# Performance work log

Hardware: AMD Instinct MI355X
Metric: run time of the kernel (lower is better)

Reference implementation:

```python
import jax, jax.numpy as jnp
import numpy as np

WIN = 8  # window_size from init_kwargs


def setup_inputs() -> dict:
    key = jax.random.key(0)
    k1, k2, k3 = jax.random.split(key, 3)
    B, H, W, C = 8, 128, 128, 384
    x = jax.random.normal(k1, (B, H * W, C), dtype=jnp.float32)
    w_qkv = jax.random.normal(k2, (C, 3 * C), dtype=jnp.float32) * 0.02
    b_qkv = jnp.zeros((3 * C,), dtype=jnp.float32)
    w_proj = jax.random.normal(k3, (C, C), dtype=jnp.float32) * 0.02
    b_proj = jnp.zeros((C,), dtype=jnp.float32)
    return {"x": x, "w_qkv": w_qkv, "b_qkv": b_qkv,
            "w_proj": w_proj, "b_proj": b_proj, "h": H, "w": W}


def reference(x, w_qkv, b_qkv, w_proj, b_proj, h, w):
    B = x.shape[0]
    C = x.shape[-1]
    win = WIN
    xs = x.reshape(B, h, w, C)
    pad_h = (-h) % win
    pad_w = (-w) % win
    xp = jnp.pad(xs, ((0, 0), (0, pad_h), (0, pad_w), (0, 0)))
    hp, wp = h + pad_h, w + pad_w
    xw = xp.reshape(B, hp // win, win, wp // win, win, C)
    xw = xw.transpose(0, 1, 3, 2, 4, 5).reshape(B, -1, win * win, C)
    qkv = xw @ w_qkv + b_qkv
    q, k, v = jnp.split(qkv, 3, axis=-1)
    # NOTE: original has no 1/sqrt(d) scaling and no head split (num_heads unused)
    attn = jax.nn.softmax(jnp.einsum('bnqc,bnkc->bnqk', q, k), axis=-1)
    out = jnp.einsum('bnqk,bnkc->bnqc', attn, v)
    out = out @ w_proj + b_proj
    # reverse window partition
    out = out.reshape(B, hp // win, wp // win, win, win, C)
    out = out.transpose(0, 1, 3, 2, 4, 5).reshape(B, hp, wp, C)
    out = out[:, :h, :w, :].reshape(B, h * w, C)
    return out
```

## Files before the change

### kernel.cpp

```cpp
#include <hip/hip_runtime.h>
#include <stdint.h>

typedef unsigned short u16;
typedef __attribute__((ext_vector_type(8))) short bf16x8;
typedef __attribute__((ext_vector_type(4))) short bf16x4;
typedef __attribute__((ext_vector_type(4))) float f32x4;

#define MFMA(A,B,C) __builtin_amdgcn_mfma_f32_16x16x32_bf16((A),(B),(C),0,0,0)

__device__ __forceinline__ u16 f2bf(float f) {
  uint32_t u = __float_as_uint(f);
  return (u16)((u + 0x7fffu + ((u >> 16) & 1u)) >> 16);
}

__device__ __forceinline__ void async16(u16* lds, const u16* g) {
  __builtin_amdgcn_global_load_lds(
      (const __attribute__((address_space(1))) uint32_t*)g,
      (__attribute__((address_space(3))) uint32_t*)lds, 16, 0, 0);
}

__global__ void k_prep(const float* __restrict__ wqkv, const float* __restrict__ wproj,
                       u16* __restrict__ wqkvP, u16* __restrict__ wprojT)
{
  int i = blockIdx.x * 256 + threadIdx.x;
  if (i < 384 * 1152) {
    int kg = i / 9216; int rem = i - kg * 9216; int n = rem >> 3; int t = rem & 7;
    wqkvP[i] = (u16)f2bf(wqkv[(kg * 8 + t) * 1152 + n]);
  }
  if (i < 384 * 384) {
    int co = i / 384, c = i - co * 384;
    wprojT[i] = (u16)f2bf(wproj[c * 384 + co]);
  }
}

__global__ __launch_bounds__(512, 4)
void k_qkv(const float* __restrict__ x, const u16* __restrict__ wp,
           const float* __restrict__ bqkv,
           u16* __restrict__ Qb, u16* __restrict__ Kbuf, u16* __restrict__ Vt)
{
  __shared__ alignas(16) u16 sA[64 * 392];
  const int tid = threadIdx.x;
  const int win = blockIdx.x;
  const int bb = win >> 8, wy = (win >> 4) & 15, wx = win & 15;

  {
    int r = tid >> 3, c0 = (tid & 7) * 48;
    int tok = (wy * 8 + (r >> 3)) * 128 + wx * 8 + (r & 7);
    const float* src = x + (size_t)(bb * 16384 + tok) * 384 + c0;
    u16* dst = &sA[r * 392 + c0];
#pragma unroll
    for (int j = 0; j < 6; ++j) {
      f32x4 a0 = *(const f32x4*)(src + j * 8);
      f32x4 a1 = *(const f32x4*)(src + j * 8 + 4);
      bf16x8 w;
#pragma unroll
      for (int e = 0; e < 4; ++e) { w[e] = (short)f2bf(a0[e]); w[e + 4] = (short)f2bf(a1[e]); }
      *(bf16x8*)(dst + j * 8) = w;
    }
  }
  __syncthreads();

  const int lane = tid & 63, l15 = lane & 15, l4 = lane >> 4;
  const int wn = tid >> 6;
  const u16* bB = wp + l4 * 9216 + (size_t)(wn * 48 + l15) * 8;
  const f32x4 z4 = {0.f, 0.f, 0.f, 0.f};

#pragma unroll
  for (int nt = 0; nt < 3; ++nt) {
    f32x4 acc[4][3];
#pragma unroll
    for (int mf = 0; mf < 4; ++mf)
#pragma unroll
      for (int nf = 0; nf < 3; ++nf) acc[mf][nf] = z4;
    const u16* bp = bB + nt * 3072;

    if (nt < 2) {
#pragma unroll
      for (int t = 0; t < 12; ++t) {
        bf16x8 af[4], bfr[3];
#pragma unroll
        for (int mf = 0; mf < 4; ++mf)
          af[mf] = *(const bf16x8*)&sA[(mf * 16 + l15) * 392 + t * 32 + l4 * 8];
#pragma unroll
        for (int nf = 0; nf < 3; ++nf)
          bfr[nf] = *(const bf16x8*)(bp + (size_t)t * 36864 + nf * 128);
#pragma unroll
        for (int mf = 0; mf < 4; ++mf)
#pragma unroll
          for (int nf = 0; nf < 3; ++nf)
            acc[mf][nf] = MFMA(bfr[nf], af[mf], acc[mf][nf]);
      }
      u16* dst = (nt == 0) ? Qb : Kbuf;
      f32x4 bias[3];
#pragma unroll
      for (int nf = 0; nf < 3; ++nf)
        bias[nf] = *(const f32x4*)&bqkv[nt * 384 + wn * 48 + nf * 16 + l4 * 4];
#pragma unroll
      for (int mf = 0; mf < 4; ++mf) {
        int row = mf * 16 + l15;
        char* rp = (char*)(dst + (size_t)(win * 64 + row) * 384);
        int sw = (nt == 1) ? ((row & 7) << 4) : 0;
#pragma unroll
        for (int nf = 0; nf < 3; ++nf) {
          bf16x4 pk;
#pragma unroll
          for (int e = 0; e < 4; ++e) pk[e] = (short)f2bf(acc[mf][nf][e] + bias[nf][e]);
          *(bf16x4*)(rp + ((wn * 96 + nf * 32 + l4 * 8) ^ sw)) = pk;
        }
      }
    } else {
#pragma unroll
      for (int t = 0; t < 12; ++t) {
        bf16x8 af[4], bfr[3];
#pragma unroll
        for (int mf = 0; mf < 4; ++mf)
          af[mf] = *(const bf16x8*)&sA[(mf * 16 + l15) * 392 + t * 32 + l4 * 8];
#pragma unroll
        for (int nf = 0; nf < 3; ++nf)
          bfr[nf] = *(const bf16x8*)(bp + (size_t)t * 36864 + nf * 128);
#pragma unroll
        for (int mf = 0; mf < 4; ++mf)
#pragma unroll
          for (int nf = 0; nf < 3; ++nf)
            acc[mf][nf] = MFMA(af[mf], bfr[nf], acc[mf][nf]);
      }
      float bv[3];
#pragma unroll
      for (int nf = 0; nf < 3; ++nf) bv[nf] = bqkv[768 + wn * 48 + nf * 16 + l15];
#pragma unroll
      for (int mf = 0; mf < 4; ++mf) {
        int key = mf * 16 + l4 * 4;
#pragma unroll
        for (int nf = 0; nf < 3; ++nf) {
          int c = wn * 48 + nf * 16 + l15;
          bf16x4 pk;
#pragma unroll
          for (int e = 0; e < 4; ++e) pk[e] = (short)f2bf(acc[mf][nf][e] + bv[nf]);
          *(bf16x4*)&Vt[((size_t)win * 384 + c) * 64 + key] = pk;
        }
      }
    }
  }
}

__global__ __launch_bounds__(256, 2)
void k_attn(const u16* __restrict__ Qb, const u16* __restrict__ Kbuf,
            const u16* __restrict__ Vt, const u16* __restrict__ WpT,
            const float* __restrict__ bproj, float* __restrict__ out)
{
  __shared__ alignas(16) u16 sKO[64 * 392];
  __shared__ alignas(16) u16 sP[64 * 64];
  __shared__ float sD[64];
  const int win = blockIdx.x;
  const int tid = threadIdx.x, wid = tid >> 6;
  const int lane = tid & 63, l15 = lane & 15, l4 = lane >> 4;
  const int swz = (l15 & 7) << 4;
  const f32x4 z4 = {0.f, 0.f, 0.f, 0.f};

  bf16x8 qa[12];
  const u16* qp = Qb + (size_t)(win * 64 + wid * 16 + l15) * 384 + l4 * 8;
#pragma unroll
  for (int cb = 0; cb < 12; ++cb) qa[cb] = *(const bf16x8*)(qp + cb * 32);
  bf16x8 vfr[6][2];
  const u16* vp = Vt + ((size_t)win * 384 + wid * 96 + l15) * 64 + l4 * 8;
#pragma unroll
  for (int nf = 0; nf < 6; ++nf)
#pragma unroll
    for (int ks = 0; ks < 2; ++ks)
      vfr[nf][ks] = *(const bf16x8*)(vp + nf * 1024 + ks * 32);
  const u16* kg = Kbuf + (size_t)win * 64 * 384;
#pragma unroll
  for (int t = 0; t < 12; ++t)
    async16((u16*)sKO + (t * 256 + tid) * 8, kg + (size_t)(t * 256 + tid) * 8);
  __syncthreads();

  f32x4 s[4];
#pragma unroll
  for (int nf = 0; nf < 4; ++nf) s[nf] = z4;
#pragma unroll
  for (int cb = 0; cb < 12; ++cb) {
#pragma unroll
    for (int nf = 0; nf < 4; ++nf) {
      bf16x8 kf = *(const bf16x8*)((char*)sKO +
                    (((nf * 16 + l15) * 768 + cb * 64 + l4 * 16) ^ swz));
      s[nf] = MFMA(kf, qa[cb], s[nf]);
    }
  }
  float mx = s[0][0];
#pragma unroll
  for (int nf = 0; nf < 4; ++nf)
#pragma unroll
    for (int e = 0; e < 4; ++e) mx = fmaxf(mx, s[nf][e]);
  mx = fmaxf(mx, __shfl_xor(mx, 16, 64));
  mx = fmaxf(mx, __shfl_xor(mx, 32, 64));
  float p[4][4], sum = 0.f;
#pragma unroll
  for (int nf = 0; nf < 4; ++nf)
#pragma unroll
    for (int e = 0; e < 4; ++e) { p[nf][e] = __expf(s[nf][e] - mx); sum += p[nf][e]; }
  sum += __shfl_xor(sum, 16, 64);
  sum += __shfl_xor(sum, 32, 64);
  const int q1 = wid * 16 + l15;
  if (lane < 16) sD[q1] = sum;
#pragma unroll
  for (int nf = 0; nf < 4; ++nf) {
    bf16x4 pk;
#pragma unroll
    for (int e = 0; e < 4; ++e) pk[e] = (short)f2bf(p[nf][e]);
    *(bf16x4*)((char*)sP + ((q1 * 128 + nf * 32 + l4 * 8) ^ swz)) = pk;
  }
  __syncthreads();

  bf16x8 pa[4][2];
#pragma unroll
  for (int mf = 0; mf < 4; ++mf)
#pragma unroll
    for (int ks = 0; ks < 2; ++ks)
      pa[mf][ks] = *(const bf16x8*)((char*)sP +
                     (((mf * 16 + l15) * 128 + ks * 64 + l4 * 16) ^ swz));
  f32x4 o[6][4];
#pragma unroll
  for (int nf = 0; nf < 6; ++nf)
#pragma unroll
    for (int mf = 0; mf < 4; ++mf) o[nf][mf] = z4;
#pragma unroll
  for (int nf = 0; nf < 6; ++nf)
#pragma unroll
    for (int ks = 0; ks < 2; ++ks)
#pragma unroll
      for (int mf = 0; mf < 4; ++mf)
        o[nf][mf] = MFMA(vfr[nf][ks], pa[mf][ks], o[nf][mf]);
#pragma unroll
  for (int nf = 0; nf < 6; ++nf)
#pragma unroll
    for (int mf = 0; mf < 4; ++mf) {
      bf16x4 pk;
#pragma unroll
      for (int e = 0; e < 4; ++e) pk[e] = (short)f2bf(o[nf][mf][e]);
      *(bf16x4*)((char*)sKO + ((mf * 16 + l15) * 784 + wid * 192 + nf * 32 + l4 * 8)) = pk;
    }
  __syncthreads();

  f32x4 pacc[6][4];
#pragma unroll
  for (int mf = 0; mf < 6; ++mf)
#pragma unroll
    for (int nf = 0; nf < 4; ++nf) pacc[mf][nf] = z4;
  const u16* wptr = WpT + (size_t)(wid * 96 + l15) * 384 + l4 * 8;
#pragma unroll
  for (int cb = 0; cb < 12; ++cb) {
    bf16x8 ob[4];
#pragma unroll
    for (int nf = 0; nf < 4; ++nf)
      ob[nf] = *(const bf16x8*)((char*)sKO + ((nf * 16 + l15) * 784 + cb * 64 + l4 * 16));
#pragma unroll
    for (int mf = 0; mf < 6; ++mf) {
      bf16x8 wf = *(const bf16x8*)(wptr + mf * 6144 + cb * 32);
#pragma unroll
      for (int nf = 0; nf < 4; ++nf)
        pacc[mf][nf] = MFMA(wf, ob[nf], pacc[mf][nf]);
    }
  }
  float rD[4];
#pragma unroll
  for (int nf = 0; nf < 4; ++nf) rD[nf] = 1.0f / sD[nf * 16 + l15];
  f32x4 bias[6];
#pragma unroll
  for (int mf = 0; mf < 6; ++mf) bias[mf] = *(const f32x4*)&bproj[wid * 96 + mf * 16 + l4 * 4];
  int bb = win >> 8, wy = (win >> 4) & 15, wx = win & 15;
#pragma unroll
  for (int nf = 0; nf < 4; ++nf) {
    int q = nf * 16 + l15;
    int tok = (wy * 8 + (q >> 3)) * 128 + wx * 8 + (q & 7);
    float* dst = out + (size_t)(bb * 16384 + tok) * 384 + wid * 96 + l4 * 4;
#pragma unroll
    for (int mf = 0; mf < 6; ++mf) {
      f32x4 v;
#pragma unroll
      for (int e = 0; e < 4; ++e) v[e] = pacc[mf][nf][e] * rD[nf] + bias[mf][e];
      *(f32x4*)(dst + mf * 16) = v;
    }
  }
}

extern "C" void kernel_launch(void* const* d_in, const int* in_sizes, int n_in,
                              void* d_out, int out_size, void* d_ws, size_t ws_size,
                              hipStream_t stream) {
  const float* x     = (const float*)d_in[0];
  const float* wqkv  = (const float*)d_in[1];
  const float* bqkv  = (const float*)d_in[2];
  const float* wproj = (const float*)d_in[3];
  const float* bproj = (const float*)d_in[4];
  float* out = (float*)d_out;
  const int Bn = in_sizes[0] / (16384 * 384);
  const size_t M = (size_t)Bn * 16384;
  const int nwin = Bn * 256;

  u16* Qb     = (u16*)d_ws;
  u16* Kbuf   = Qb + M * 384;
  u16* Vt     = Kbuf + M * 384;
  u16* WqkvP  = Vt + M * 384;
  u16* WprojT = WqkvP + (size_t)384 * 1152;

  k_prep<<<dim3((384 * 1152 + 255) / 256), dim3(256), 0, stream>>>(wqkv, wproj, WqkvP, WprojT);
  k_qkv<<<dim3(nwin), dim3(512), 0, stream>>>(x, WqkvP, bqkv, Qb, Kbuf, Vt);
  k_attn<<<dim3(nwin), dim3(256), 0, stream>>>(Qb, Kbuf, Vt, WprojT, bproj, out);
}
```

Measured before the change: 613.2 us.

## Fuse QKV projection, window attention and output projection into one kernel

Merges the QKV GEMM kernel and the attention+projection kernel into a single per-window kernel that keeps Q, K, V, P and O in LDS and registers instead of round-tripping bf16 Q/K/V through global memory. It also software-prefetches weight fragments one k-step ahead and computes Q and K in one combined loop. The aim is to remove the intermediate HBM writes and reads and one launch. In exchange, the kernel needs 144 KB of dynamic LDS per block, which limits occupancy to about one block per CU, and only half the waves do the score/softmax stage.

```diff
diff --git a/kernel.cpp b/kernel.cpp
--- a/kernel.cpp
+++ b/kernel.cpp
@@ -11,12 +11,6 @@
 __device__ __forceinline__ u16 f2bf(float f) {
   uint32_t u = __float_as_uint(f);
   return (u16)((u + 0x7fffu + ((u >> 16) & 1u)) >> 16);
-}
-
-__device__ __forceinline__ void async16(u16* lds, const u16* g) {
-  __builtin_amdgcn_global_load_lds(
-      (const __attribute__((address_space(1))) uint32_t*)g,
-      (__attribute__((address_space(3))) uint32_t*)lds, 16, 0, 0);
 }
 
 __global__ void k_prep(const float* __restrict__ wqkv, const float* __restrict__ wproj,
@@ -33,21 +27,30 @@
   }
 }
 
-__global__ __launch_bounds__(512, 4)
-void k_qkv(const float* __restrict__ x, const u16* __restrict__ wp,
-           const float* __restrict__ bqkv,
-           u16* __restrict__ Qb, u16* __restrict__ Kbuf, u16* __restrict__ Vt)
+__global__ __launch_bounds__(512, 2)
+void k_fused(const float* __restrict__ x, const u16* __restrict__ wp,
+             const float* __restrict__ bqkv, const u16* __restrict__ WpT,
+             const float* __restrict__ bproj, float* __restrict__ out)
 {
-  __shared__ alignas(16) u16 sA[64 * 392];
+  extern __shared__ char smem[];
+  char* sX = smem;
+  char* sQ = smem + 49152;
+  char* sK = smem + 98304;
+  float* sD = (float*)(smem + 8192);
+
   const int tid = threadIdx.x;
   const int win = blockIdx.x;
   const int bb = win >> 8, wy = (win >> 4) & 15, wx = win & 15;
+  const int lane = tid & 63, l15 = lane & 15, l4 = lane >> 4;
+  const int wn = tid >> 6;
+  const int swz = (l15 & 7) << 4;
+  const f32x4 z4 = {0.f, 0.f, 0.f, 0.f};
 
   {
     int r = tid >> 3, c0 = (tid & 7) * 48;
     int tok = (wy * 8 + (r >> 3)) * 128 + wx * 8 + (r & 7);
     const float* src = x + (size_t)(bb * 16384 + tok) * 384 + c0;
-    u16* dst = &sA[r * 392 + c0];
+    int rb = r * 768, sw = (r & 7) << 4;
 #pragma unroll
     for (int j = 0; j < 6; ++j) {
       f32x4 a0 = *(const f32x4*)(src + j * 8);
@@ -55,230 +58,254 @@
       bf16x8 w;
 #pragma unroll
       for (int e = 0; e < 4; ++e) { w[e] = (short)f2bf(a0[e]); w[e + 4] = (short)f2bf(a1[e]); }
-      *(bf16x8*)(dst + j * 8) = w;
-    }
+      *(bf16x8*)(sX + ((rb + c0 * 2 + j * 16) ^ sw)) = w;
+    }
+  }
+
+  const u16* bB = wp + l4 * 9216 + (size_t)(wn * 48 + l15) * 8;
+  bf16x8 bq[3], bk[3], nbq[3], nbk[3];
+#pragma unroll
+  for (int nf = 0; nf < 3; ++nf) {
+    bq[nf] = *(const bf16x8*)(bB + nf * 128);
+    bk[nf] = *(const bf16x8*)(bB + 3072 + nf * 128);
   }
   __syncthreads();
 
-  const int lane = tid & 63, l15 = lane & 15, l4 = lane >> 4;
-  const int wn = tid >> 6;
-  const u16* bB = wp + l4 * 9216 + (size_t)(wn * 48 + l15) * 8;
-  const f32x4 z4 = {0.f, 0.f, 0.f, 0.f};
-
-#pragma unroll
-  for (int nt = 0; nt < 3; ++nt) {
-    f32x4 acc[4][3];
+  f32x4 aq[4][3], ak[4][3];
+#pragma unroll
+  for (int mf = 0; mf < 4; ++mf)
+#pragma unroll
+    for (int nf = 0; nf < 3; ++nf) { aq[mf][nf] = z4; ak[mf][nf] = z4; }
+#pragma unroll
+  for (int t = 0; t < 12; ++t) {
+    if (t < 11) {
+#pragma unroll
+      for (int nf = 0; nf < 3; ++nf) {
+        nbq[nf] = *(const bf16x8*)(bB + (size_t)(t + 1) * 36864 + nf * 128);
+        nbk[nf] = *(const bf16x8*)(bB + (size_t)(t + 1) * 36864 + 3072 + nf * 128);
+      }
+    }
+    bf16x8 af[4];
 #pragma unroll
     for (int mf = 0; mf < 4; ++mf)
-#pragma unroll
-      for (int nf = 0; nf < 3; ++nf) acc[mf][nf] = z4;
-    const u16* bp = bB + nt * 3072;
-
-    if (nt < 2) {
-#pragma unroll
-      for (int t = 0; t < 12; ++t) {
-        bf16x8 af[4], bfr[3];
+      af[mf] = *(const bf16x8*)(sX + (((mf * 16 + l15) * 768 + t * 64 + l4 * 16) ^ swz));
+#pragma unroll
+    for (int mf = 0; mf < 4; ++mf)
+#pragma unroll
+      for (int nf = 0; nf < 3; ++nf) {
+        aq[mf][nf] = MFMA(bq[nf], af[mf], aq[mf][nf]);
+        ak[mf][nf] = MFMA(bk[nf], af[mf], ak[mf][nf]);
+      }
+    if (t < 11) {
+#pragma unroll
+      for (int nf = 0; nf < 3; ++nf) { bq[nf] = nbq[nf]; bk[nf] = nbk[nf]; }
+    }
+  }
+  {
+    f32x4 biasq[3], biask[3];
+#pragma unroll
+    for (int nf = 0; nf < 3; ++nf) {
+      biasq[nf] = *(const f32x4*)&bqkv[wn * 48 + nf * 16 + l4 * 4];
+      biask[nf] = *(const f32x4*)&bqkv[384 + wn * 48 + nf * 16 + l4 * 4];
+    }
+#pragma unroll
+    for (int mf = 0; mf < 4; ++mf) {
+      int rb = (mf * 16 + l15) * 768;
+#pragma unroll
+      for (int nf = 0; nf < 3; ++nf) {
+        bf16x4 pq, pk_;
+#pragma unroll
+        for (int e = 0; e < 4; ++e) {
+          pq[e]  = (short)f2bf(aq[mf][nf][e] + biasq[nf][e]);
+          pk_[e] = (short)f2bf(ak[mf][nf][e] + biask[nf][e]);
+        }
+        *(bf16x4*)(sQ + ((rb + wn * 96 + nf * 32 + l4 * 8) ^ swz)) = pq;
+        *(bf16x4*)(sK + ((rb + wn * 96 + nf * 32 + l4 * 8) ^ swz)) = pk_;
+      }
+    }
+  }
+
+  f32x4 av[4][3];
+#pragma unroll
+  for (int mf = 0; mf < 4; ++mf)
+#pragma unroll
+    for (int nf = 0; nf < 3; ++nf) av[mf][nf] = z4;
+  {
+    bf16x8 bv[3], nbv[3];
+#pragma unroll
+    for (int nf = 0; nf < 3; ++nf) bv[nf] = *(const bf16x8*)(bB + 6144 + nf * 128);
+#pragma unroll
+    for (int t = 0; t < 12; ++t) {
+      if (t < 11) {
+#pragma unroll
+        for (int nf = 0; nf < 3; ++nf)
+          nbv[nf] = *(const bf16x8*)(bB + (size_t)(t + 1) * 36864 + 6144 + nf * 128);
+      }
+      bf16x8 af[4];
+#pragma unroll
+      for (int mf = 0; mf < 4; ++mf)
+        af[mf] = *(const bf16x8*)(sX + (((mf * 16 + l15) * 768 + t * 64 + l4 * 16) ^ swz));
+#pragma unroll
+      for (int mf = 0; mf < 4; ++mf)
+#pragma unroll
+        for (int nf = 0; nf < 3; ++nf)
+          av[mf][nf] = MFMA(af[mf], bv[nf], av[mf][nf]);
+      if (t < 11) {
+#pragma unroll
+        for (int nf = 0; nf < 3; ++nf) bv[nf] = nbv[nf];
+      }
+    }
+  }
+  bf16x8 vfr[3][2];
+  {
+    float bvv[3];
+#pragma unroll
+    for (int nf = 0; nf < 3; ++nf) bvv[nf] = bqkv[768 + wn * 48 + nf * 16 + l15];
+#pragma unroll
+    for (int nf = 0; nf < 3; ++nf)
+#pragma unroll
+      for (int g = 0; g < 2; ++g) {
+        bf16x8 w;
+#pragma unroll
+        for (int e = 0; e < 4; ++e) {
+          w[e]     = (short)f2bf(av[2 * g][nf][e] + bvv[nf]);
+          w[e + 4] = (short)f2bf(av[2 * g + 1][nf][e] + bvv[nf]);
+        }
+        vfr[nf][g] = w;
+      }
+  }
+  __syncthreads();
+
+  if ((wn & 1) == 0) {
+    const int qt = wn >> 1;
+    f32x4 s[4];
+#pragma unroll
+    for (int nf = 0; nf < 4; ++nf) s[nf] = z4;
+#pragma unroll
+    for (int cb = 0; cb < 12; ++cb) {
+      bf16x8 qa = *(const bf16x8*)(sQ + (((qt * 16 + l15) * 768 + cb * 64 + l4 * 16) ^ swz));
+#pragma unroll
+      for (int nf = 0; nf < 4; ++nf) {
+        bf16x8 kf = *(const bf16x8*)(sK + (((nf * 16 + l15) * 768 + cb * 64 + l4 * 16) ^ swz));
+        s[nf] = MFMA(kf, qa, s[nf]);
+      }
+    }
+    float mx = s[0][0];
+#pragma unroll
+    for (int nf = 0; nf < 4; ++nf)
+#pragma unroll
+      for (int e = 0; e < 4; ++e) mx = fmaxf(mx, s[nf][e]);
+    mx = fmaxf(mx, __shfl_xor(mx, 16, 64));
+    mx = fmaxf(mx, __shfl_xor(mx, 32, 64));
+    float p[4][4], sum = 0.f;
+#pragma unroll
+    for (int nf = 0; nf < 4; ++nf)
+#pragma unroll
+      for (int e = 0; e < 4; ++e) { p[nf][e] = __expf(s[nf][e] - mx); sum += p[nf][e]; }
+    sum += __shfl_xor(sum, 16, 64);
+    sum += __shfl_xor(sum, 32, 64);
+    const int q1 = qt * 16 + l15;
+    if (l4 == 0) sD[q1] = sum;
+#pragma unroll
+    for (int nf = 0; nf < 4; ++nf) {
+      bf16x4 w;
+#pragma unroll
+      for (int e = 0; e < 4; ++e) w[e] = (short)f2bf(p[nf][e]);
+      *(bf16x4*)(sX + ((q1 * 128 + nf * 32 + l4 * 8) ^ swz)) = w;
+    }
+  }
+  __syncthreads();
+
+  {
+    bf16x8 pa[4][2];
+#pragma unroll
+    for (int mf = 0; mf < 4; ++mf) {
+      int qb = (mf * 16 + l15) * 128;
+#pragma unroll
+      for (int g = 0; g < 2; ++g) {
+        bf16x4 lo = *(const bf16x4*)(sX + ((qb + (2 * g) * 32 + l4 * 8) ^ swz));
+        bf16x4 hi = *(const bf16x4*)(sX + ((qb + (2 * g + 1) * 32 + l4 * 8) ^ swz));
+        bf16x8 w;
+#pragma unroll
+        for (int e = 0; e < 4; ++e) { w[e] = lo[e]; w[e + 4] = hi[e]; }
+        pa[mf][g] = w;
+      }
+    }
+    f32x4 o[3][4];
+#pragma unroll
+    for (int nf = 0; nf < 3; ++nf)
+#pragma unroll
+      for (int mf = 0; mf < 4; ++mf) o[nf][mf] = z4;
+#pragma unroll
+    for (int nf = 0; nf < 3; ++nf)
+#pragma unroll
+      for (int g = 0; g < 2; ++g)
 #pragma unroll
         for (int mf = 0; mf < 4; ++mf)
-          af[mf] = *(const bf16x8*)&sA[(mf * 16 + l15) * 392 + t * 32 + l4 * 8];
-#pragma unroll
-        for (int nf = 0; nf < 3; ++nf)
-          bfr[nf] = *(const bf16x8*)(bp + (size_t)t * 36864 + nf * 128);
-#pragma unroll
-        for (int mf = 0; mf < 4; ++mf)
-#pragma unroll
-          for (int nf = 0; nf < 3; ++nf)
-            acc[mf][nf] = MFMA(bfr[nf], af[mf], acc[mf][nf]);
-      }
-      u16* dst = (nt == 0) ? Qb : Kbuf;
-      f32x4 bias[3];
-#pragma unroll
-      for (int nf = 0; nf < 3; ++nf)
-        bias[nf] = *(const f32x4*)&bqkv[nt * 384 + wn * 48 + nf * 16 + l4 * 4];
-#pragma unroll
-      for (int mf = 0; mf < 4; ++mf) {
-        int row = mf * 16 + l15;
-        char* rp = (char*)(dst + (size_t)(win * 64 + row) * 384);
-        int sw = (nt == 1) ? ((row & 7) << 4) : 0;
-#pragma unroll
-        for (int nf = 0; nf < 3; ++nf) {
-          bf16x4 pk;
-#pragma unroll
-          for (int e = 0; e < 4; ++e) pk[e] = (short)f2bf(acc[mf][nf][e] + bias[nf][e]);
-          *(bf16x4*)(rp + ((wn * 96 + nf * 32 + l4 * 8) ^ sw)) = pk;
-        }
-      }
-    } else {
-#pragma unroll
-      for (int t = 0; t < 12; ++t) {
-        bf16x8 af[4], bfr[3];
-#pragma unroll
-        for (int mf = 0; mf < 4; ++mf)
-          af[mf] = *(const bf16x8*)&sA[(mf * 16 + l15) * 392 + t * 32 + l4 * 8];
-#pragma unroll
-        for (int nf = 0; nf < 3; ++nf)
-          bfr[nf] = *(const bf16x8*)(bp + (size_t)t * 36864 + nf * 128);
-#pragma unroll
-        for (int mf = 0; mf < 4; ++mf)
-#pragma unroll
-          for (int nf = 0; nf < 3; ++nf)
-            acc[mf][nf] = MFMA(af[mf], bfr[nf], acc[mf][nf]);
-      }
-      float bv[3];
-#pragma unroll
-      for (int nf = 0; nf < 3; ++nf) bv[nf] = bqkv[768 + wn * 48 + nf * 16 + l15];
-#pragma unroll
-      for (int mf = 0; mf < 4; ++mf) {
-        int key = mf * 16 + l4 * 4;
-#pragma unroll
-        for (int nf = 0; nf < 3; ++nf) {
-          int c = wn * 48 + nf * 16 + l15;
-          bf16x4 pk;
-#pragma unroll
-          for (int e = 0; e < 4; ++e) pk[e] = (short)f2bf(acc[mf][nf][e] + bv[nf]);
-          *(bf16x4*)&Vt[((size_t)win * 384 + c) * 64 + key] = pk;
-        }
-      }
-    }
-  }
-}
-
-__global__ __launch_bounds__(256, 2)
-void k_attn(const u16* __restrict__ Qb, const u16* __restrict__ Kbuf,
-            const u16* __restrict__ Vt, const u16* __restrict__ WpT,
-            const float* __restrict__ bproj, float* __restrict__ out)
-{
-  __shared__ alignas(16) u16 sKO[64 * 392];
-  __shared__ alignas(16) u16 sP[64 * 64];
-  __shared__ float sD[64];
-  const int win = blockIdx.x;
-  const int tid = threadIdx.x, wid = tid >> 6;
-  const int lane = tid & 63, l15 = lane & 15, l4 = lane >> 4;
-  const int swz = (l15 & 7) << 4;
-  const f32x4 z4 = {0.f, 0.f, 0.f, 0.f};
-
-  bf16x8 qa[12];
-  const u16* qp = Qb + (size_t)(win * 64 + wid * 16 + l15) * 384 + l4 * 8;
-#pragma unroll
-  for (int cb = 0; cb < 12; ++cb) qa[cb] = *(const bf16x8*)(qp + cb * 32);
-  bf16x8 vfr[6][2];
-  const u16* vp = Vt + ((size_t)win * 384 + wid * 96 + l15) * 64 + l4 * 8;
-#pragma unroll
-  for (int nf = 0; nf < 6; ++nf)
-#pragma unroll
-    for (int ks = 0; ks < 2; ++ks)
-      vfr[nf][ks] = *(const bf16x8*)(vp + nf * 1024 + ks * 32);
-  const u16* kg = Kbuf + (size_t)win * 64 * 384;
-#pragma unroll
-  for (int t = 0; t < 12; ++t)
-    async16((u16*)sKO + (t * 256 + tid) * 8, kg + (size_t)(t * 256 + tid) * 8);
+          o[nf][mf] = MFMA(vfr[nf][g], pa[mf][g], o[nf][mf]);
+#pragma unroll
+    for (int mf = 0; mf < 4; ++mf) {
+      int rb = (mf * 16 + l15) * 768;
+#pragma unroll
+      for (int nf = 0; nf < 3; ++nf) {
+        bf16x4 w;
+#pragma unroll
+        for (int e = 0; e < 4; ++e) w[e] = (short)f2bf(o[nf][mf][e]);
+        *(bf16x4*)(sQ + ((rb + wn * 96 + nf * 32 + l4 * 8) ^ swz)) = w;
+      }
+    }
+  }
   __syncthreads();
 
-  f32x4 s[4];
-#pragma unroll
-  for (int nf = 0; nf < 4; ++nf) s[nf] = z4;
-#pragma unroll
-  for (int cb = 0; cb < 12; ++cb) {
+  {
+    f32x4 pacc[3][4];
+#pragma unroll
+    for (int mf = 0; mf < 3; ++mf)
+#pragma unroll
+      for (int nf = 0; nf < 4; ++nf) pacc[mf][nf] = z4;
+    const u16* wptr = WpT + (size_t)(wn * 48 + l15) * 384 + l4 * 8;
+    bf16x8 wf[3], nwf[3];
+#pragma unroll
+    for (int mf = 0; mf < 3; ++mf) wf[mf] = *(const bf16x8*)(wptr + mf * 6144);
+#pragma unroll
+    for (int cb = 0; cb < 12; ++cb) {
+      if (cb < 11) {
+#pragma unroll
+        for (int mf = 0; mf < 3; ++mf)
+          nwf[mf] = *(const bf16x8*)(wptr + mf * 6144 + (cb + 1) * 32);
+      }
+      bf16x8 ob[4];
+#pragma unroll
+      for (int nf = 0; nf < 4; ++nf)
+        ob[nf] = *(const bf16x8*)(sQ + (((nf * 16 + l15) * 768 + cb * 64 + l4 * 16) ^ swz));
+#pragma unroll
+      for (int mf = 0; mf < 3; ++mf)
+#pragma unroll
+        for (int nf = 0; nf < 4; ++nf)
+          pacc[mf][nf] = MFMA(wf[mf], ob[nf], pacc[mf][nf]);
+      if (cb < 11) {
+#pragma unroll
+        for (int mf = 0; mf < 3; ++mf) wf[mf] = nwf[mf];
+      }
+    }
+    float rD[4];
+#pragma unroll
+    for (int nf = 0; nf < 4; ++nf) rD[nf] = 1.0f / sD[nf * 16 + l15];
+    f32x4 bias[3];
+#pragma unroll
+    for (int mf = 0; mf < 3; ++mf) bias[mf] = *(const f32x4*)&bproj[wn * 48 + mf * 16 + l4 * 4];
 #pragma unroll
     for (int nf = 0; nf < 4; ++nf) {
-      bf16x8 kf = *(const bf16x8*)((char*)sKO +
-                    (((nf * 16 + l15) * 768 + cb * 64 + l4 * 16) ^ swz));
-      s[nf] = MFMA(kf, qa[cb], s[nf]);
-    }
-  }
-  float mx = s[0][0];
-#pragma unroll
-  for (int nf = 0; nf < 4; ++nf)
-#pragma unroll
-    for (int e = 0; e < 4; ++e) mx = fmaxf(mx, s[nf][e]);
-  mx = fmaxf(mx, __shfl_xor(mx, 16, 64));
-  mx = fmaxf(mx, __shfl_xor(mx, 32, 64));
-  float p[4][4], sum = 0.f;
-#pragma unroll
-  for (int nf = 0; nf < 4; ++nf)
-#pragma unroll
-    for (int e = 0; e < 4; ++e) { p[nf][e] = __expf(s[nf][e] - mx); sum += p[nf][e]; }
-  sum += __shfl_xor(sum, 16, 64);
-  sum += __shfl_xor(sum, 32, 64);
-  const int q1 = wid * 16 + l15;
-  if (lane < 16) sD[q1] = sum;
-#pragma unroll
-  for (int nf = 0; nf < 4; ++nf) {
-    bf16x4 pk;
-#pragma unroll
-    for (int e = 0; e < 4; ++e) pk[e] = (short)f2bf(p[nf][e]);
-    *(bf16x4*)((char*)sP + ((q1 * 128 + nf * 32 + l4 * 8) ^ swz)) = pk;
-  }
-  __syncthreads();
-
-  bf16x8 pa[4][2];
-#pragma unroll
-  for (int mf = 0; mf < 4; ++mf)
-#pragma unroll
-    for (int ks = 0; ks < 2; ++ks)
-      pa[mf][ks] = *(const bf16x8*)((char*)sP +
-                     (((mf * 16 + l15) * 128 + ks * 64 + l4 * 16) ^ swz));
-  f32x4 o[6][4];
-#pragma unroll
-  for (int nf = 0; nf < 6; ++nf)
-#pragma unroll
-    for (int mf = 0; mf < 4; ++mf) o[nf][mf] = z4;
-#pragma unroll
-  for (int nf = 0; nf < 6; ++nf)
-#pragma unroll
-    for (int ks = 0; ks < 2; ++ks)
-#pragma unroll
-      for (int mf = 0; mf < 4; ++mf)
-        o[nf][mf] = MFMA(vfr[nf][ks], pa[mf][ks], o[nf][mf]);
-#pragma unroll
-  for (int nf = 0; nf < 6; ++nf)
-#pragma unroll
-    for (int mf = 0; mf < 4; ++mf) {
-      bf16x4 pk;
-#pragma unroll
-      for (int e = 0; e < 4; ++e) pk[e] = (short)f2bf(o[nf][mf][e]);
-      *(bf16x4*)((char*)sKO + ((mf * 16 + l15) * 784 + wid * 192 + nf * 32 + l4 * 8)) = pk;
-    }
-  __syncthreads();
-
-  f32x4 pacc[6][4];
-#pragma unroll
-  for (int mf = 0; mf < 6; ++mf)
-#pragma unroll
-    for (int nf = 0; nf < 4; ++nf) pacc[mf][nf] = z4;
-  const u16* wptr = WpT + (size_t)(wid * 96 + l15) * 384 + l4 * 8;
-#pragma unroll
-  for (int cb = 0; cb < 12; ++cb) {
-    bf16x8 ob[4];
-#pragma unroll
-    for (int nf = 0; nf < 4; ++nf)
-      ob[nf] = *(const bf16x8*)((char*)sKO + ((nf * 16 + l15) * 784 + cb * 64 + l4 * 16));
-#pragma unroll
-    for (int mf = 0; mf < 6; ++mf) {
-      bf16x8 wf = *(const bf16x8*)(wptr + mf * 6144 + cb * 32);
-#pragma unroll
-      for (int nf = 0; nf < 4; ++nf)
-        pacc[mf][nf] = MFMA(wf, ob[nf], pacc[mf][nf]);
-    }
-  }
-  float rD[4];
-#pragma unroll
-  for (int nf = 0; nf < 4; ++nf) rD[nf] = 1.0f / sD[nf * 16 + l15];
-  f32x4 bias[6];
-#pragma unroll
-  for (int mf = 0; mf < 6; ++mf) bias[mf] = *(const f32x4*)&bproj[wid * 96 + mf * 16 + l4 * 4];
-  int bb = win >> 8, wy = (win >> 4) & 15, wx = win & 15;
-#pragma unroll
-  for (int nf = 0; nf < 4; ++nf) {
-    int q = nf * 16 + l15;
-    int tok = (wy * 8 + (q >> 3)) * 128 + wx * 8 + (q & 7);
-    float* dst = out + (size_t)(bb * 16384 + tok) * 384 + wid * 96 + l4 * 4;
-#pragma unroll
-    for (int mf = 0; mf < 6; ++mf) {
-      f32x4 v;
-#pragma unroll
-      for (int e = 0; e < 4; ++e) v[e] = pacc[mf][nf][e] * rD[nf] + bias[mf][e];
-      *(f32x4*)(dst + mf * 16) = v;
+      int q = nf * 16 + l15;
+      int tok = (wy * 8 + (q >> 3)) * 128 + wx * 8 + (q & 7);
+      float* dst = out + (size_t)(bb * 16384 + tok) * 384 + wn * 48 + l4 * 4;
+#pragma unroll
+      for (int mf = 0; mf < 3; ++mf) {
+        f32x4 v;
+#pragma unroll
+        for (int e = 0; e < 4; ++e) v[e] = pacc[mf][nf][e] * rD[nf] + bias[mf][e];
+        *(f32x4*)(dst + mf * 16) = v;
+      }
     }
   }
 }
@@ -293,16 +320,14 @@
   const float* bproj = (const float*)d_in[4];
   float* out = (float*)d_out;
   const int Bn = in_sizes[0] / (16384 * 384);
-  const size_t M = (size_t)Bn * 16384;
   const int nwin = Bn * 256;
 
-  u16* Qb     = (u16*)d_ws;
-  u16* Kbuf   = Qb + M * 384;
-  u16* Vt     = Kbuf + M * 384;
-  u16* WqkvP  = Vt + M * 384;
+  u16* WqkvP  = (u16*)d_ws;
   u16* WprojT = WqkvP + (size_t)384 * 1152;
 
+  (void)hipFuncSetAttribute((const void*)k_fused,
+                            hipFuncAttributeMaxDynamicSharedMemorySize, 147456);
+
   k_prep<<<dim3((384 * 1152 + 255) / 256), dim3(256), 0, stream>>>(wqkv, wproj, WqkvP, WprojT);
-  k_qkv<<<dim3(nwin), dim3(512), 0, stream>>>(x, WqkvP, bqkv, Qb, Kbuf, Vt);
-  k_attn<<<dim3(nwin), dim3(256), 0, stream>>>(Qb, Kbuf, Vt, WprojT, bproj, out);
+  k_fused<<<dim3(nwin), dim3(512), 147456, stream>>>(x, WqkvP, bqkv, WprojT, bproj, out);
 }
```

After: 562.4 us. 8.3% less time.
